# Optimization experiments

Hardware: AMD Instinct MI355X
Metric: run time of the kernel (lower is better)

Reference implementation:

```python
import jax, jax.numpy as jnp
import numpy as np

D_MODEL = 768
NUM_HEADS = 12
HEAD_DIM = D_MODEL // NUM_HEADS


def setup_inputs() -> dict:
    key = jax.random.key(0)
    ks = jax.random.split(key, 9)
    B, S = 2, 2048
    s = 1.0 / np.sqrt(D_MODEL)
    x = jax.random.normal(ks[0], (B, S, D_MODEL), dtype=jnp.float32)
    Wq = jax.random.normal(ks[1], (D_MODEL, D_MODEL), dtype=jnp.float32) * s
    Wk = jax.random.normal(ks[2], (D_MODEL, D_MODEL), dtype=jnp.float32) * s
    Wv = jax.random.normal(ks[3], (D_MODEL, D_MODEL), dtype=jnp.float32) * s
    Wo = jax.random.normal(ks[4], (D_MODEL, D_MODEL), dtype=jnp.float32) * s
    bq = jax.random.normal(ks[5], (D_MODEL,), dtype=jnp.float32) * 0.01
    bk = jax.random.normal(ks[6], (D_MODEL,), dtype=jnp.float32) * 0.01
    bv = jax.random.normal(ks[7], (D_MODEL,), dtype=jnp.float32) * 0.01
    bo = jax.random.normal(ks[8], (D_MODEL,), dtype=jnp.float32) * 0.01
    return {"x": x, "Wq": Wq, "bq": bq, "Wk": Wk, "bk": bk,
            "Wv": Wv, "bv": bv, "Wo": Wo, "bo": bo}


def reference(x, Wq, bq, Wk, bk, Wv, bv, Wo, bo):
    B, S, _ = x.shape
    # projections; reshape to [B, H, S, Dh]
    def split_heads(t):
        return t.reshape(B, S, NUM_HEADS, HEAD_DIM).transpose(0, 2, 1, 3)
    q = split_heads(x @ Wq + bq)
    k = split_heads(x @ Wk + bk)
    v = split_heads(x @ Wv + bv)
    scale = 1.0 / np.sqrt(HEAD_DIM)
    scores = jnp.einsum("bhqd,bhkd->bhqk", q, k) * scale  # [B,H,S,S]
    attn = jax.nn.softmax(scores, axis=-1)
    # dropout p=0.0 (eval) -> identity
    ctx = jnp.einsum("bhqk,bhkd->bhqd", attn, v)
    ctx = ctx.transpose(0, 2, 1, 3).reshape(B, S, D_MODEL)
    return ctx @ Wo + bo
```

## Files before the change

kernel.cpp:

```cpp
#include <hip/hip_runtime.h>
#include <hip/hip_bf16.h>
#include <hip/hip_fp16.h>

#define D_MODEL 768
#define NHEADS  12
#define HD      64
#define BATCH   2
#define SEQ     2048
#define NTOK    (BATCH*SEQ)
#define NX      ((size_t)NTOK * D_MODEL)
#define NW      ((size_t)D_MODEL * D_MODEL)
#define NBH     (BATCH*NHEADS)
#define SC_LOG2 0.18033688f

typedef __attribute__((ext_vector_type(8))) short    short8;
typedef __attribute__((ext_vector_type(8))) _Float16 half8;
typedef __attribute__((ext_vector_type(2))) __fp16   fp16x2;
typedef __attribute__((ext_vector_type(4))) float    f32x4;

__device__ __forceinline__ float bf2f(short s) {
    union { unsigned u; float f; } c;
    c.u = ((unsigned)(unsigned short)s) << 16;
    return c.f;
}
__device__ __forceinline__ short f2bf(float f) {
    __hip_bfloat16 h = __float2bfloat16(f);
    return *(short*)&h;
}

#ifdef __has_builtin
#if __has_builtin(__builtin_amdgcn_global_load_lds)
#define HAS_GLD 1
#endif
#if __has_builtin(__builtin_amdgcn_exp2f)
#define EXP2(x) __builtin_amdgcn_exp2f(x)
#else
#define EXP2(x) exp2f(x)
#endif
#if __has_builtin(__builtin_amdgcn_cvt_pkrtz)
#define HAS_PKRTZ 1
#endif
#else
#define EXP2(x) exp2f(x)
#endif
#ifdef HAS_GLD
#define GLD16(gp, lp) __builtin_amdgcn_global_load_lds( \
    (const __attribute__((address_space(1))) void*)(gp), \
    (__attribute__((address_space(3))) void*)(lp), 16, 0, 0)
#endif

#ifdef HAS_PKRTZ
#define PKF16(a, b) __builtin_amdgcn_cvt_pkrtz((a), (b))
#else
#define PKF16(a, b) ((fp16x2){ (__fp16)(a), (__fp16)(b) })
#endif

__global__ __launch_bounds__(256) void fused_conv(
        const void* __restrict__ xin,
        const void* __restrict__ w0, const void* __restrict__ w1,
        const void* __restrict__ w2, const void* __restrict__ w3,
        const void* __restrict__ b0, const void* __restrict__ b1,
        const void* __restrict__ b2, const void* __restrict__ b3,
        short* __restrict__ xc, short* __restrict__ wt,
        short* __restrict__ bc, int* __restrict__ flag)
{
    __shared__ int red[256];
    __shared__ float T[64][65];
    const int tid = threadIdx.x;
    const int F = blockIdx.x;

    {
        const short* xs = (const short*)xin;
        int maxe = 0;
#pragma unroll
        for (int u = 0; u < 16; ++u) {
            int e = ((unsigned short)xs[tid * 16 + u] >> 7) & 0xFF;
            maxe = max(maxe, e);
        }
        red[tid] = maxe;
        __syncthreads();
        for (int s = 128; s > 0; s >>= 1) {
            if (tid < s) red[tid] = max(red[tid], red[tid + s]);
            __syncthreads();
        }
    }
    const bool isf = (red[0] > 140);

    if (F < 3072) {
        const int i = F * 256 + tid;
        if (isf) {
            float4 f = ((const float4*)xin)[i];
            short4 o = { f2bf(f.x), f2bf(f.y), f2bf(f.z), f2bf(f.w) };
            ((short4*)xc)[i] = o;
        } else {
            ((short4*)xc)[i] = ((const short4*)xin)[i];
        }
    } else if (F < 3648) {
        const int G = F - 3072;
        const int z = G / 144, rr = G % 144;
        const int k0 = (rr % 12) * 64, n0 = (rr / 12) * 64;
        const void* src = (z == 0) ? w0 : (z == 1) ? w1 : (z == 2) ? w2 : w3;
        const float sc = (z == 0) ? SC_LOG2 : 1.0f;
        const int la = tid & 15, lb = tid >> 4;
#pragma unroll
        for (int u = 0; u < 4; ++u) {
            const int kr = (lb & 3) + 4 * u + 16 * (lb >> 2);
            if (isf) {
                float4 f = *(const float4*)((const float*)src + (size_t)(k0 + kr) * D_MODEL + n0 + la * 4);
                T[kr][la*4+0] = f.x; T[kr][la*4+1] = f.y; T[kr][la*4+2] = f.z; T[kr][la*4+3] = f.w;
            } else {
                short4 s = *(const short4*)((const short*)src + (size_t)(k0 + kr) * D_MODEL + n0 + la * 4);
                T[kr][la*4+0] = bf2f(s.x); T[kr][la*4+1] = bf2f(s.y);
                T[kr][la*4+2] = bf2f(s.z); T[kr][la*4+3] = bf2f(s.w);
            }
        }
        __syncthreads();
#pragma unroll
        for (int u = 0; u < 4; ++u) {
            const int nr = (lb & 3) + 4 * u + 16 * (lb >> 2);
            short4 o = { f2bf(T[la*4+0][nr] * sc), f2bf(T[la*4+1][nr] * sc),
                         f2bf(T[la*4+2][nr] * sc), f2bf(T[la*4+3][nr] * sc) };
            *(short4*)(wt + (size_t)z * NW + (size_t)(n0 + nr) * D_MODEL + k0 + la * 4) = o;
        }
    } else {
        if (tid == 0) *flag = isf ? 1 : 0;
        const void* srcs[4] = { b0, b1, b2, b3 };
        for (int z = 0; z < 4; ++z) {
            const float sc = (z == 0) ? SC_LOG2 : 1.0f;
            for (int i = tid; i < D_MODEL; i += 256) {
                float v = isf ? ((const float*)srcs[z])[i] : bf2f(((const short*)srcs[z])[i]);
                bc[z * D_MODEL + i] = f2bf(v * sc);
            }
        }
    }
}

__global__ __launch_bounds__(256) void qkv_gemm(const short* __restrict__ X,
                                                const short* __restrict__ Wt,
                                                const short* __restrict__ bias,
                                                short* __restrict__ qb,
                                                short* __restrict__ kb,
                                                _Float16* __restrict__ Vt)
{
    __shared__ __align__(16) char shbuf[24576];
    short* Als = (short*)shbuf;
    short* Bls = (short*)(shbuf + 8192);
    _Float16* T = (_Float16*)shbuf;

    const int tid = threadIdx.x;
    const int wave = tid >> 6, lane = tid & 63;
    const int quad = lane >> 4, l16 = lane & 15;
    const int wm = wave & 1, wn = wave >> 1;
    const int m0 = blockIdx.x * 64;
    const int ng = blockIdx.y * 128;

    f32x4 acc[2][4];
#pragma unroll
    for (int nt = 0; nt < 4; ++nt) {
        const float bv = bf2f(bias[ng + wn*64 + nt*16 + l16]);
#pragma unroll
        for (int mt = 0; mt < 2; ++mt) acc[mt][nt] = (f32x4){bv, bv, bv, bv};
    }

    const int row = tid >> 2, ch = (tid & 3) * 8;
#ifdef HAS_GLD
#define QSTAGE(buf, k0) do { \
        GLD16(X  + (size_t)(m0 + row)      * D_MODEL + (k0) + ch, &Als[(buf)*2048 + tid*8]); \
        GLD16(Wt + (size_t)(ng + row)      * D_MODEL + (k0) + ch, &Bls[(buf)*4096 + tid*8]); \
        GLD16(Wt + (size_t)(ng + 64 + row) * D_MODEL + (k0) + ch, &Bls[(buf)*4096 + 2048 + tid*8]); \
    } while (0)
#else
#define QSTAGE(buf, k0) do { \
        short8 r0 = *(const short8*)(X  + (size_t)(m0 + row)      * D_MODEL + (k0) + ch); \
        short8 r2 = *(const short8*)(Wt + (size_t)(ng + row)      * D_MODEL + (k0) + ch); \
        short8 r3 = *(const short8*)(Wt + (size_t)(ng + 64 + row) * D_MODEL + (k0) + ch); \
        *(short8*)&Als[(buf)*2048 + tid*8] = r0; \
        *(short8*)&Bls[(buf)*4096 + tid*8] = r2; \
        *(short8*)&Bls[(buf)*4096 + 2048 + tid*8] = r3; \
    } while (0)
#endif

    QSTAGE(0, 0);
    __syncthreads();

    for (int ks = 0; ks < 24; ++ks) {
        const int cur = ks & 1;
        if (ks + 1 < 24) QSTAGE(cur ^ 1, (ks + 1) * 32);

        short8 a[2], b[4];
#pragma unroll
        for (int mt = 0; mt < 2; ++mt)
            a[mt] = *(const short8*)&Als[cur*2048 + (wm*32 + mt*16 + l16) * 32 + quad*8];
#pragma unroll
        for (int nt = 0; nt < 4; ++nt)
            b[nt] = *(const short8*)&Bls[cur*4096 + (wn*64 + nt*16 + l16) * 32 + quad*8];
#pragma unroll
        for (int mt = 0; mt < 2; ++mt)
#pragma unroll
        for (int nt = 0; nt < 4; ++nt)
            acc[mt][nt] = __builtin_amdgcn_mfma_f32_16x16x32_bf16(a[mt], b[nt], acc[mt][nt], 0, 0, 0);

        __syncthreads();
    }
#undef QSTAGE

    const int seg = blockIdx.y / 6;
    if (seg < 2) {
        short* out = seg ? kb : qb;
        const int nl = ng - seg * 768;
#pragma unroll
        for (int mt = 0; mt < 2; ++mt)
#pragma unroll
        for (int nt = 0; nt < 4; ++nt) {
            const int n = nl + wn*64 + nt*16 + l16;
#pragma unroll
            for (int r = 0; r < 4; ++r) {
                const int m = m0 + wm*32 + mt*16 + quad*4 + r;
                out[(size_t)m * D_MODEL + n] = f2bf(acc[mt][nt][r]);
            }
        }
    } else {
        const int batch = m0 >> 11, tokb = m0 & (SEQ - 1);
#pragma unroll
        for (int nt = 0; nt < 4; ++nt) {
            const int dim_l = wn*64 + nt*16 + l16;
#pragma unroll
            for (int mt = 0; mt < 2; ++mt) {
                const int tok_l = wm*32 + mt*16 + quad*4;
                union { _Float16 h4[4]; int2 v; } u;
#pragma unroll
                for (int r = 0; r < 4; ++r) u.h4[r] = (_Float16)acc[mt][nt][r];
                *(int2*)&T[dim_l * 72 + tok_l] = u.v;
            }
        }
        __syncthreads();
#pragma unroll
        for (int u = 0; u < 4; ++u) {
            const int slot = tid + u * 256;
            const int drow = slot >> 3, chk = slot & 7;
            int4 val = *(const int4*)&T[drow * 72 + chk * 8];
            const int dim_g = ng - 1536 + drow;
            const int h = dim_g >> 6, d = dim_g & 63;
            *(int4*)(Vt + ((size_t)(batch * NHEADS + h) * HD + d) * SEQ + tokb + chk*8) = val;
        }
    }
}

__global__ __launch_bounds__(256) void out_gemm(const short* __restrict__ X,
                                                const short* __restrict__ Wt,
                                                const short* __restrict__ bias,
                                                void* __restrict__ outv,
                                                const int* __restrict__ flag)
{
    __shared__ short Als[2][2048];
    __shared__ short Bls[2][2048];

    const int tid = threadIdx.x;
    const int wave = tid >> 6, lane = tid & 63;
    const int quad = lane >> 4, l16 = lane & 15;
    const int m0 = blockIdx.x * 64;
    const int n0 = blockIdx.y * 64;

    f32x4 acc[4];
#pragma unroll
    for (int nt = 0; nt < 4; ++nt) {
        const float bv = bf2f(bias[n0 + nt*16 + l16]);
        acc[nt] = (f32x4){bv, bv, bv, bv};
    }

    const int row = tid >> 2, ch = (tid & 3) * 8;
#ifdef HAS_GLD
#define OSTAGE(buf, k0) do { \
        GLD16(X  + (size_t)(m0 + row) * D_MODEL + (k0) + ch, &Als[buf][tid*8]); \
        GLD16(Wt + (size_t)(n0 + row) * D_MODEL + (k0) + ch, &Bls[buf][tid*8]); \
    } while (0)
#else
#define OSTAGE(buf, k0) do { \
        short8 r0 = *(const short8*)(X  + (size_t)(m0 + row) * D_MODEL + (k0) + ch); \
        short8 r1 = *(const short8*)(Wt + (size_t)(n0 + row) * D_MODEL + (k0) + ch); \
        *(short8*)&Als[buf][tid*8] = r0; \
        *(short8*)&Bls[buf][tid*8] = r1; \
    } while (0)
#endif

    OSTAGE(0, 0);
    __syncthreads();

    for (int ks = 0; ks < 24; ++ks) {
        const int cur = ks & 1;
        if (ks + 1 < 24) OSTAGE(cur ^ 1, (ks + 1) * 32);

        short8 a = *(const short8*)&Als[cur][(wave*16 + l16) * 32 + quad*8];
#pragma unroll
        for (int nt = 0; nt < 4; ++nt) {
            short8 b = *(const short8*)&Bls[cur][(nt*16 + l16) * 32 + quad*8];
            acc[nt] = __builtin_amdgcn_mfma_f32_16x16x32_bf16(a, b, acc[nt], 0, 0, 0);
        }
        __syncthreads();
    }
#undef OSTAGE

    const bool outf32 = (*flag != 0);
#pragma unroll
    for (int nt = 0; nt < 4; ++nt) {
        const int n = n0 + nt*16 + l16;
#pragma unroll
        for (int r = 0; r < 4; ++r) {
            const int m = m0 + wave*16 + quad*4 + r;
            const size_t idx = (size_t)m * D_MODEL + n;
            if (outf32) ((float*)outv)[idx] = acc[nt][r];
            else        ((short*)outv)[idx] = f2bf(acc[nt][r]);
        }
    }
}

__global__ __launch_bounds__(256, 3) void attn_mfma(const short* __restrict__ q,
                                                    const short* __restrict__ k,
                                                    const _Float16* __restrict__ Vt,
                                                    _Float16* __restrict__ Op,
                                                    float* __restrict__ mlp)
{
    __shared__ __align__(16) short    Kls[2][4096];
    __shared__ __align__(16) _Float16 Vls[2][4096];
    __shared__ __align__(16) _Float16 Pls[4][2048];

    const int tid  = threadIdx.x;
    const int wave = tid >> 6, lane = tid & 63;
    const int quad = lane >> 4, l16 = lane & 15;

    const int F = blockIdx.x;
    const int xcd = F & 7, slot = F >> 3;
    const int bh = xcd * 3 + (slot >> 5);
    const int rem = slot & 31;
    const int q0 = (rem >> 1) * 128;
    const int sp = rem & 1;
    const int kb0 = sp * (SEQ / 2);
    const int b = bh / NHEADS, h = bh % NHEADS;
    const size_t bS = (size_t)b * SEQ;

    short8 qf[2][2];
#pragma unroll
    for (int col = 0; col < 2; ++col)
#pragma unroll
    for (int k0h = 0; k0h < 2; ++k0h)
        qf[col][k0h] = *(const short8*)(q + (bS + q0 + wave*32 + col*16 + l16) * D_MODEL
                                          + h*HD + k0h*32 + quad*8);

    half8 ones;
#pragma unroll
    for (int j = 0; j < 8; ++j) ones[j] = (_Float16)1.0f;

    const int cK0 = tid >> 6,       keyK0 = tid & 63;
    const int cK1 = (tid + 256) >> 6, keyK1 = tid & 63;
    const short* kgp0 = k + (bS + kb0 + keyK0) * D_MODEL + h*HD + cK0*8;
    const short* kgp1 = k + (bS + kb0 + keyK1) * D_MODEL + h*HD + cK1*8;
    const _Float16* vgp0 = Vt + ((size_t)bh * HD + keyK0) * SEQ + kb0 + cK0*8;
    const _Float16* vgp1 = Vt + ((size_t)bh * HD + keyK1) * SEQ + kb0 + cK1*8;

#ifdef HAS_GLD
#define STAGE_K(buf, j0) do { \
        GLD16(kgp0 + (size_t)(j0) * D_MODEL, &Kls[buf][tid*8]); \
        GLD16(kgp1 + (size_t)(j0) * D_MODEL, &Kls[buf][(tid+256)*8]); \
    } while (0)
#define STAGE_V(buf, j0) do { \
        GLD16(vgp0 + (j0), &Vls[buf][tid*8]); \
        GLD16(vgp1 + (j0), &Vls[buf][(tid+256)*8]); \
    } while (0)
#else
#define STAGE_K(buf, j0) do { \
        short8 a_ = *(const short8*)(kgp0 + (size_t)(j0) * D_MODEL); \
        short8 b_ = *(const short8*)(kgp1 + (size_t)(j0) * D_MODEL); \
        *(short8*)&Kls[buf][tid*8] = a_;  *(short8*)&Kls[buf][(tid+256)*8] = b_; \
    } while (0)
#define STAGE_V(buf, j0) do { \
        half8 c_ = *(const half8*)(vgp0 + (j0)); \
        half8 d_ = *(const half8*)(vgp1 + (j0)); \
        *(half8*)&Vls[buf][tid*8] = c_;  *(half8*)&Vls[buf][(tid+256)*8] = d_; \
    } while (0)
#endif

    float m_ = -1e30f;
    f32x4 laccA = (f32x4){0.f,0.f,0.f,0.f}, laccB = (f32x4){0.f,0.f,0.f,0.f};
    f32x4 o[4][2];
#pragma unroll
    for (int t = 0; t < 4; ++t) { o[t][0] = (f32x4){0.f,0.f,0.f,0.f}; o[t][1] = (f32x4){0.f,0.f,0.f,0.f}; }

    f32x4 sA[4][2], sB[4][2];

#define NT (SEQ / 2 / 64)

#define QK(S, KB) do { \
    _Pragma("unroll") \
    for (int t = 0; t < 4; ++t) { S[t][0] = (f32x4){0.f,0.f,0.f,0.f}; S[t][1] = (f32x4){0.f,0.f,0.f,0.f}; } \
    __builtin_amdgcn_s_setprio(1); \
    _Pragma("unroll") \
    for (int k0h = 0; k0h < 2; ++k0h) \
    _Pragma("unroll") \
    for (int t = 0; t < 4; ++t) { \
        short8 kf = *(const short8*)&Kls[KB][(k0h*4 + quad)*512 + (t*16 + l16)*8]; \
        S[t][0] = __builtin_amdgcn_mfma_f32_16x16x32_bf16(kf, qf[0][k0h], S[t][0], 0, 0, 0); \
        S[t][1] = __builtin_amdgcn_mfma_f32_16x16x32_bf16(kf, qf[1][k0h], S[t][1], 0, 0, 0); \
    } \
    __builtin_amdgcn_s_setprio(0); \
} while (0)

#define BODY(JT, SCUR, SNXT) do { \
    if ((JT) + 2 < NT) STAGE_K(((JT) + 2) & 1, ((JT) + 2) * 64); \
    if ((JT) + 1 < NT) { \
        STAGE_V(((JT) + 1) & 1, ((JT) + 1) * 64); \
        QK(SNXT, ((JT) + 1) & 1); \
    } \
    { \
         \
        float mx = SCUR[0][0][0]; \
        _Pragma("unroll") \
        for (int t = 0; t < 4; ++t) \
        _Pragma("unroll") \
        for (int c = 0; c < 2; ++c) \
        _Pragma("unroll") \
        for (int r = 0; r < 4; ++r) mx = fmaxf(mx, SCUR[t][c][r]); \
        if (__any(mx > m_ + 8.f)) { \
            _Pragma("unroll") \
            for (int d = 1; d < 64; d <<= 1) mx = fmaxf(mx, __shfl_xor(mx, d)); \
            const float mn = fmaxf(m_, mx); \
            const float al = EXP2(m_ - mn); \
            _Pragma("unroll") \
            for (int t = 0; t < 4; ++t) \
            _Pragma("unroll") \
            for (int c = 0; c < 2; ++c) { \
                o[t][c][0] *= al; o[t][c][1] *= al; o[t][c][2] *= al; o[t][c][3] *= al; \
            } \
            laccA[0] *= al; laccB[0] *= al; \
            m_ = mn; \
        } \
         \
        _Pragma("unroll") \
        for (int t = 0; t < 4; ++t) \
        _Pragma("unroll") \
        for (int c = 0; c < 2; ++c) { \
            union { fp16x2 h2[2]; int2 v; } u4; \
            u4.h2[0] = PKF16(EXP2(SCUR[t][c][0] - m_), EXP2(SCUR[t][c][1] - m_)); \
            u4.h2[1] = PKF16(EXP2(SCUR[t][c][2] - m_), EXP2(SCUR[t][c][3] - m_)); \
            const int kc = 2*t + (quad >> 1); \
            *(int2*)&Pls[wave][c*1024 + kc*128 + l16*8 + (quad & 1)*4] = u4.v; \
        } \
         \
        const int vb = (JT) & 1; \
        __builtin_amdgcn_s_setprio(1); \
        _Pragma("unroll") \
        for (int k0h = 0; k0h < 2; ++k0h) { \
            half8 pf0 = *(half8*)&Pls[wave][(k0h*4 + quad)*128 + l16*8]; \
            half8 pf1 = *(half8*)&Pls[wave][1024 + (k0h*4 + quad)*128 + l16*8]; \
            laccA = __builtin_amdgcn_mfma_f32_16x16x32_f16(ones, pf0, laccA, 0, 0, 0); \
            laccB = __builtin_amdgcn_mfma_f32_16x16x32_f16(ones, pf1, laccB, 0, 0, 0); \
            _Pragma("unroll") \
            for (int t = 0; t < 4; ++t) { \
                half8 vf = *(const half8*)&Vls[vb][(k0h*4 + quad)*512 + (t*16 + l16)*8]; \
                o[t][0] = __builtin_amdgcn_mfma_f32_16x16x32_f16(vf, pf0, o[t][0], 0, 0, 0); \
                o[t][1] = __builtin_amdgcn_mfma_f32_16x16x32_f16(vf, pf1, o[t][1], 0, 0, 0); \
            } \
        } \
        __builtin_amdgcn_s_setprio(0); \
    } \
    __syncthreads(); \
} while (0)

    STAGE_K(0, 0); STAGE_V(0, 0);
    __syncthreads();
    STAGE_K(1, 64);
    QK(sA, 0);
    __syncthreads();

    for (int jt = 0; jt < NT; jt += 2) {
        BODY(jt,     sA, sB);
        BODY(jt + 1, sB, sA);
    }

#pragma unroll
    for (int col = 0; col < 2; ++col) {
        const f32x4 la = col ? laccB : laccA;
        const float inv = 1.0f / la[0];
        const int myq = q0 + wave*32 + col*16 + l16;
        const size_t prow = ((size_t)sp * (NBH * SEQ) + (size_t)bh * SEQ + myq);
        _Float16* orow = Op + prow * HD;
#pragma unroll
        for (int t = 0; t < 4; ++t) {
            union { _Float16 h4[4]; int2 v; } u4;
#pragma unroll
            for (int r = 0; r < 4; ++r) u4.h4[r] = (_Float16)(o[t][col][r] * inv);
            *(int2*)(orow + t*16 + quad*4) = u4.v;
        }
        if (quad == 0) {
            float2 mlv; mlv.x = m_; mlv.y = la[0];
            *(float2*)&mlp[prow * 2] = mlv;
        }
    }
#undef BODY
#undef QK
#undef NT
#undef STAGE_K
#undef STAGE_V
}

__global__ __launch_bounds__(256) void attn_combine(const _Float16* __restrict__ Op,
                                                    const float* __restrict__ mlp,
                                                    short* __restrict__ ctx)
{
    const int gid = blockIdx.x * 256 + threadIdx.x;
    const int r = gid >> 3, seg = gid & 7;
    const float2 a  = *(const float2*)&mlp[(size_t)r * 2];
    const float2 c2 = *(const float2*)&mlp[((size_t)(NBH * SEQ) + r) * 2];
    const float M  = fmaxf(a.x, c2.x);
    const float w1 = EXP2(a.x - M) * a.y;
    const float w2 = EXP2(c2.x - M) * c2.y;
    const float inv = 1.0f / (w1 + w2);
    const half8 o1 = *(const half8*)&Op[(size_t)r * HD + seg * 8];
    const half8 o2 = *(const half8*)&Op[(size_t)(NBH * SEQ) * HD + (size_t)r * HD + seg * 8];
    union { short s[8]; int4 v; } u;
#pragma unroll
    for (int j = 0; j < 8; ++j)
        u.s[j] = f2bf((w1 * (float)o1[j] + w2 * (float)o2[j]) * inv);
    const int bh = r >> 11, qq = r & (SEQ - 1);
    const int bb = bh / NHEADS, hh = bh % NHEADS;
    *(int4*)&ctx[((size_t)(bb * SEQ + qq)) * D_MODEL + hh * HD + seg * 8] = u.v;
}

extern "C" void kernel_launch(void* const* d_in, const int* in_sizes, int n_in,
                              void* d_out, int out_size, void* d_ws, size_t ws_size,
                              hipStream_t stream)
{
    int* flag = (int*)d_ws;
    short* xc = (short*)((char*)d_ws + 64);
    short* Wt = xc + NX;
    short* bc = Wt + 4 * NW;
    short* qb = bc + 4 * D_MODEL;
    short* kb = qb + NX;
    _Float16* Vt = (_Float16*)(kb + NX);
    short* cb = (short*)(Vt + NX);
    _Float16* Op = (_Float16*)(cb + NX);
    float* mlp = (float*)(Op + (size_t)2 * NBH * SEQ * HD);

    fused_conv<<<3649, 256, 0, stream>>>(d_in[0],
                                         d_in[1], d_in[3], d_in[5], d_in[7],
                                         d_in[2], d_in[4], d_in[6], d_in[8],
                                         xc, Wt, bc, flag);

    qkv_gemm<<<dim3(NTOK/64, 2304/128), 256, 0, stream>>>(xc, Wt, bc, qb, kb, Vt);

    attn_mfma<<<768, 256, 0, stream>>>(qb, kb, Vt, Op, mlp);

    attn_combine<<<1536, 256, 0, stream>>>(Op, mlp, cb);

    out_gemm<<<dim3(NTOK/64, D_MODEL/64), 256, 0, stream>>>(cb, Wt + 3*NW, bc + 3*D_MODEL, d_out, flag);
}
```

Baseline: 195.9 us.

## Reorder attention pipeline to issue QK of next tile with PV of current

Splits the loop body into QK, PV and SOFTMAX macros and reschedules each iteration. The QK MFMAs for tile j+1 and the PV MFMAs for tile j now run as one high-priority burst, followed by the softmax of tile j+1, which writes P for the next iteration. This replaces the sA/sB register double buffer and the 2x unrolled loop with a single scores buffer per iteration. The aim is a long uninterrupted MFMA stream and lower register pressure. The risk is that softmax exp work is no longer hidden between MFMA phases, and the loop is less unrolled.

```diff
diff --git a/kernel.cpp b/kernel.cpp
--- a/kernel.cpp
+++ b/kernel.cpp
@@ -350,7 +350,7 @@
 #pragma unroll
     for (int j = 0; j < 8; ++j) ones[j] = (_Float16)1.0f;
 
-    const int cK0 = tid >> 6,       keyK0 = tid & 63;
+    const int cK0 = tid >> 6,         keyK0 = tid & 63;
     const int cK1 = (tid + 256) >> 6, keyK1 = tid & 63;
     const short* kgp0 = k + (bS + kb0 + keyK0) * D_MODEL + h*HD + cK0*8;
     const short* kgp1 = k + (bS + kb0 + keyK1) * D_MODEL + h*HD + cK1*8;
@@ -385,14 +385,11 @@
 #pragma unroll
     for (int t = 0; t < 4; ++t) { o[t][0] = (f32x4){0.f,0.f,0.f,0.f}; o[t][1] = (f32x4){0.f,0.f,0.f,0.f}; }
 
-    f32x4 sA[4][2], sB[4][2];
-
 #define NT (SEQ / 2 / 64)
 
 #define QK(S, KB) do { \
     _Pragma("unroll") \
     for (int t = 0; t < 4; ++t) { S[t][0] = (f32x4){0.f,0.f,0.f,0.f}; S[t][1] = (f32x4){0.f,0.f,0.f,0.f}; } \
-    __builtin_amdgcn_s_setprio(1); \
     _Pragma("unroll") \
     for (int k0h = 0; k0h < 2; ++k0h) \
     _Pragma("unroll") \
@@ -401,80 +398,81 @@
         S[t][0] = __builtin_amdgcn_mfma_f32_16x16x32_bf16(kf, qf[0][k0h], S[t][0], 0, 0, 0); \
         S[t][1] = __builtin_amdgcn_mfma_f32_16x16x32_bf16(kf, qf[1][k0h], S[t][1], 0, 0, 0); \
     } \
-    __builtin_amdgcn_s_setprio(0); \
 } while (0)
 
-#define BODY(JT, SCUR, SNXT) do { \
-    if ((JT) + 2 < NT) STAGE_K(((JT) + 2) & 1, ((JT) + 2) * 64); \
-    if ((JT) + 1 < NT) { \
-        STAGE_V(((JT) + 1) & 1, ((JT) + 1) * 64); \
-        QK(SNXT, ((JT) + 1) & 1); \
+#define PV(VB) do { \
+    _Pragma("unroll") \
+    for (int k0h = 0; k0h < 2; ++k0h) { \
+        half8 pf0 = *(half8*)&Pls[wave][(k0h*4 + quad)*128 + l16*8]; \
+        half8 pf1 = *(half8*)&Pls[wave][1024 + (k0h*4 + quad)*128 + l16*8]; \
+        laccA = __builtin_amdgcn_mfma_f32_16x16x32_f16(ones, pf0, laccA, 0, 0, 0); \
+        laccB = __builtin_amdgcn_mfma_f32_16x16x32_f16(ones, pf1, laccB, 0, 0, 0); \
+        _Pragma("unroll") \
+        for (int t = 0; t < 4; ++t) { \
+            half8 vf = *(const half8*)&Vls[VB][(k0h*4 + quad)*512 + (t*16 + l16)*8]; \
+            o[t][0] = __builtin_amdgcn_mfma_f32_16x16x32_f16(vf, pf0, o[t][0], 0, 0, 0); \
+            o[t][1] = __builtin_amdgcn_mfma_f32_16x16x32_f16(vf, pf1, o[t][1], 0, 0, 0); \
+        } \
     } \
-    { \
-         \
-        float mx = SCUR[0][0][0]; \
+} while (0)
+
+#define SOFTMAX(S) do { \
+    float mx = S[0][0][0]; \
+    _Pragma("unroll") \
+    for (int t = 0; t < 4; ++t) \
+    _Pragma("unroll") \
+    for (int c = 0; c < 2; ++c) \
+    _Pragma("unroll") \
+    for (int r = 0; r < 4; ++r) mx = fmaxf(mx, S[t][c][r]); \
+    if (__any(mx > m_ + 8.f)) { \
         _Pragma("unroll") \
-        for (int t = 0; t < 4; ++t) \
-        _Pragma("unroll") \
-        for (int c = 0; c < 2; ++c) \
-        _Pragma("unroll") \
-        for (int r = 0; r < 4; ++r) mx = fmaxf(mx, SCUR[t][c][r]); \
-        if (__any(mx > m_ + 8.f)) { \
-            _Pragma("unroll") \
-            for (int d = 1; d < 64; d <<= 1) mx = fmaxf(mx, __shfl_xor(mx, d)); \
-            const float mn = fmaxf(m_, mx); \
-            const float al = EXP2(m_ - mn); \
-            _Pragma("unroll") \
-            for (int t = 0; t < 4; ++t) \
-            _Pragma("unroll") \
-            for (int c = 0; c < 2; ++c) { \
-                o[t][c][0] *= al; o[t][c][1] *= al; o[t][c][2] *= al; o[t][c][3] *= al; \
-            } \
-            laccA[0] *= al; laccB[0] *= al; \
-            m_ = mn; \
-        } \
-         \
+        for (int d = 1; d < 64; d <<= 1) mx = fmaxf(mx, __shfl_xor(mx, d)); \
+        const float mn = fmaxf(m_, mx); \
+        const float al = EXP2(m_ - mn); \
         _Pragma("unroll") \
         for (int t = 0; t < 4; ++t) \
         _Pragma("unroll") \
         for (int c = 0; c < 2; ++c) { \
-            union { fp16x2 h2[2]; int2 v; } u4; \
-            u4.h2[0] = PKF16(EXP2(SCUR[t][c][0] - m_), EXP2(SCUR[t][c][1] - m_)); \
-            u4.h2[1] = PKF16(EXP2(SCUR[t][c][2] - m_), EXP2(SCUR[t][c][3] - m_)); \
-            const int kc = 2*t + (quad >> 1); \
-            *(int2*)&Pls[wave][c*1024 + kc*128 + l16*8 + (quad & 1)*4] = u4.v; \
+            o[t][c][0] *= al; o[t][c][1] *= al; o[t][c][2] *= al; o[t][c][3] *= al; \
         } \
-         \
-        const int vb = (JT) & 1; \
-        __builtin_amdgcn_s_setprio(1); \
-        _Pragma("unroll") \
-        for (int k0h = 0; k0h < 2; ++k0h) { \
-            half8 pf0 = *(half8*)&Pls[wave][(k0h*4 + quad)*128 + l16*8]; \
-            half8 pf1 = *(half8*)&Pls[wave][1024 + (k0h*4 + quad)*128 + l16*8]; \
-            laccA = __builtin_amdgcn_mfma_f32_16x16x32_f16(ones, pf0, laccA, 0, 0, 0); \
-            laccB = __builtin_amdgcn_mfma_f32_16x16x32_f16(ones, pf1, laccB, 0, 0, 0); \
-            _Pragma("unroll") \
-            for (int t = 0; t < 4; ++t) { \
-                half8 vf = *(const half8*)&Vls[vb][(k0h*4 + quad)*512 + (t*16 + l16)*8]; \
-                o[t][0] = __builtin_amdgcn_mfma_f32_16x16x32_f16(vf, pf0, o[t][0], 0, 0, 0); \
-                o[t][1] = __builtin_amdgcn_mfma_f32_16x16x32_f16(vf, pf1, o[t][1], 0, 0, 0); \
-            } \
-        } \
-        __builtin_amdgcn_s_setprio(0); \
+        laccA[0] *= al; laccB[0] *= al; \
+        m_ = mn; \
     } \
+    _Pragma("unroll") \
+    for (int t = 0; t < 4; ++t) \
+    _Pragma("unroll") \
+    for (int c = 0; c < 2; ++c) { \
+        union { fp16x2 h2[2]; int2 v; } u4; \
+        u4.h2[0] = PKF16(EXP2(S[t][c][0] - m_), EXP2(S[t][c][1] - m_)); \
+        u4.h2[1] = PKF16(EXP2(S[t][c][2] - m_), EXP2(S[t][c][3] - m_)); \
+        const int kc = 2*t + (quad >> 1); \
+        *(int2*)&Pls[wave][c*1024 + kc*128 + l16*8 + (quad & 1)*4] = u4.v; \
+    } \
+} while (0)
+
+#define BODY(JT) do { \
+    if ((JT) + 2 < NT) STAGE_K(((JT) + 2) & 1, ((JT) + 2) * 64); \
+    if ((JT) + 1 < NT) STAGE_V(((JT) + 1) & 1, ((JT) + 1) * 64); \
+    f32x4 s_[4][2]; \
+    __builtin_amdgcn_s_setprio(1); \
+    if ((JT) + 1 < NT) QK(s_, ((JT) + 1) & 1); \
+    PV((JT) & 1); \
+    __builtin_amdgcn_s_setprio(0); \
+    if ((JT) + 1 < NT) SOFTMAX(s_); \
     __syncthreads(); \
 } while (0)
 
     STAGE_K(0, 0); STAGE_V(0, 0);
     __syncthreads();
     STAGE_K(1, 64);
-    QK(sA, 0);
+    {
+        f32x4 s_[4][2];
+        QK(s_, 0);
+        SOFTMAX(s_);
+    }
     __syncthreads();
 
-    for (int jt = 0; jt < NT; jt += 2) {
-        BODY(jt,     sA, sB);
-        BODY(jt + 1, sB, sA);
-    }
+    for (int jt = 0; jt < NT; ++jt) BODY(jt);
 
 #pragma unroll
     for (int col = 0; col < 2; ++col) {
@@ -496,6 +494,8 @@
         }
     }
 #undef BODY
+#undef SOFTMAX
+#undef PV
 #undef QK
 #undef NT
 #undef STAGE_K
```

Measured after the change: 174.5 us. 10.9% less time.
